# Optimization experiments

Hardware: AMD Instinct MI355X
Metric: run time of the kernel (lower is better)

Reference implementation:

```python
import jax, jax.numpy as jnp
import numpy as np

N, D = 8192, 512
LOGIT_SCALE = 2.659


def setup_inputs() -> dict:
    key = jax.random.key(0)
    k1, k2, k3 = jax.random.split(key, 3)
    text_features = jax.random.normal(k1, (N, D), dtype=jnp.float32)
    image_features = jax.random.normal(k2, (N, D), dtype=jnp.float32)
    labels = jax.random.randint(k3, (N,), 0, 100, dtype=jnp.int64)
    # sprinkle in some -1 (unlabeled) entries like the original supports
    labels = jnp.where(jax.random.uniform(jax.random.fold_in(key, 7), (N,)) < 0.1, -1, labels)
    return {"text_features": text_features, "image_features": image_features, "labels": labels}


def _l2_normalize(x):
    n = jnp.sqrt(jnp.sum(x * x, axis=-1, keepdims=True))
    return x / jnp.maximum(n, 1e-12)


def _soft_ce(s, t):
    # -(t * log softmax(s)).sum(-1) / t.sum(-1), averaged over rows
    loss = -jnp.sum(t * jax.nn.log_softmax(s, axis=-1), axis=-1)
    return jnp.mean(loss / jnp.sum(t, axis=-1))


def reference(text_features, image_features, labels):
    img = _l2_normalize(image_features)
    txt = _l2_normalize(text_features)
    logits_per_image = LOGIT_SCALE * (img @ txt.T)   # [N, N]
    logits_per_text = LOGIT_SCALE * (txt @ img.T)    # [N, N]

    # Vectorized equivalent of the per-row loop:
    # T[i,j] = 1 if i == j else (labels[i] == labels[j] and labels[i] != -1)
    eq = (labels[:, None] == labels[None, :]) & (labels[:, None] != -1)
    n = labels.shape[0]
    target = jnp.where(jnp.eye(n, dtype=bool), 1.0, eq.astype(jnp.float32))

    return (_soft_ce(logits_per_image, target) + _soft_ce(logits_per_text, target)) / 2
```

## Files before the change

### kernel.cpp

```cpp
#include <hip/hip_runtime.h>
#include <hip/hip_bf16.h>

#define N_ROWS 8192
#define DIM 512
#define SCALE 2.659f
#define MAXLOGIT 2.659f
#define LOG2E 1.4426950408889634f
#define NCHUNK 16
#define CHUNK 512
#define BM 128
#define BN 128
#define NCLS 128

typedef __attribute__((ext_vector_type(8))) short short8;
typedef __attribute__((ext_vector_type(4))) float f32x4;

#define ZERO_F4 36896

__device__ __forceinline__ unsigned short f2bf(float f) {
    unsigned int u = __float_as_uint(f);
    u += 0x7fffu + ((u >> 16) & 1u);
    return (unsigned short)(u >> 16);
}

__global__ __launch_bounds__(256) void norm_cast_kernel(
    const float* __restrict__ text, const float* __restrict__ image,
    const int* __restrict__ labels,
    unsigned short* __restrict__ imgn, unsigned short* __restrict__ txtn,
    float4* __restrict__ zbase, float* __restrict__ sd, float* __restrict__ out)
{
    int zi = blockIdx.x * 256 + threadIdx.x;
    if (zi < ZERO_F4) zbase[zi] = make_float4(0.f, 0.f, 0.f, 0.f);
    if (zi == 0) out[0] = 0.f;

    int row  = blockIdx.x * 4 + (threadIdx.x >> 6);
    int lane = threadIdx.x & 63;
    const float4* si = (const float4*)(image + (size_t)row * DIM) + lane * 2;
    const float4* st = (const float4*)(text  + (size_t)row * DIM) + lane * 2;
    float4 a = si[0], b = si[1], c = st[0], d = st[1];
    float ssa = a.x*a.x + a.y*a.y + a.z*a.z + a.w*a.w
              + b.x*b.x + b.y*b.y + b.z*b.z + b.w*b.w;
    float sst = c.x*c.x + c.y*c.y + c.z*c.z + c.w*c.w
              + d.x*d.x + d.y*d.y + d.z*d.z + d.w*d.w;
    float sab = a.x*c.x + a.y*c.y + a.z*c.z + a.w*c.w
              + b.x*d.x + b.y*d.y + b.z*d.z + b.w*d.w;
    #pragma unroll
    for (int m = 1; m < 64; m <<= 1) {
        ssa += __shfl_xor(ssa, m, 64);
        sst += __shfl_xor(sst, m, 64);
        sab += __shfl_xor(sab, m, 64);
    }
    float sca = 1.0f / fmaxf(sqrtf(ssa), 1e-12f);
    float sct = 1.0f / fmaxf(sqrtf(sst), 1e-12f);
    uint4 oi, ot;
    oi.x = (unsigned)f2bf(a.x*sca) | ((unsigned)f2bf(a.y*sca) << 16);
    oi.y = (unsigned)f2bf(a.z*sca) | ((unsigned)f2bf(a.w*sca) << 16);
    oi.z = (unsigned)f2bf(b.x*sca) | ((unsigned)f2bf(b.y*sca) << 16);
    oi.w = (unsigned)f2bf(b.z*sca) | ((unsigned)f2bf(b.w*sca) << 16);
    ot.x = (unsigned)f2bf(c.x*sct) | ((unsigned)f2bf(c.y*sct) << 16);
    ot.y = (unsigned)f2bf(c.z*sct) | ((unsigned)f2bf(c.w*sct) << 16);
    ot.z = (unsigned)f2bf(d.x*sct) | ((unsigned)f2bf(d.y*sct) << 16);
    ot.w = (unsigned)f2bf(d.z*sct) | ((unsigned)f2bf(d.w*sct) << 16);
    *((uint4*)(imgn + (size_t)row * DIM) + lane) = oi;
    *((uint4*)(txtn + (size_t)row * DIM) + lane) = ot;
    if (lane == 0)
        sd[row] = (labels[row] < 0) ? sab * sca * sct : 0.0f;
}

__global__ __launch_bounds__(256) void class_sum_kernel(
    const unsigned short* __restrict__ imgn, const unsigned short* __restrict__ txtn,
    const int* __restrict__ labels,
    float* __restrict__ c_txt, float* __restrict__ c_img, int* __restrict__ cnt)
{
    __shared__ int list[1024];
    __shared__ int lcount;
    int blk = blockIdx.x;
    int cls = blk & (NCLS - 1);
    int mat = (blk >> 7) & 1;
    int slc = blk >> 8;
    const unsigned* src = (const unsigned*)(mat ? imgn : txtn);
    float* dst = mat ? c_img : c_txt;
    int tid = threadIdx.x;
    if (tid == 0) lcount = 0;
    __syncthreads();
    int base0 = slc * 1024;
    #pragma unroll
    for (int it = 0; it < 4; ++it) {
        int i  = base0 + it * 256 + tid;
        int lb = labels[i];
        if (lb == cls) { int s = atomicAdd(&lcount, 1); list[s] = i; }
    }
    __syncthreads();
    int m = lcount;
    if (m == 0) return;
    if (mat == 0 && tid == 0) atomicAdd(&cnt[cls], m);
    float a0 = 0.f, a1 = 0.f;
    int r = 0;
    for (; r + 4 <= m; r += 4) {
        unsigned u0 = src[(size_t)list[r]   * (DIM/2) + tid];
        unsigned u1 = src[(size_t)list[r+1] * (DIM/2) + tid];
        unsigned u2 = src[(size_t)list[r+2] * (DIM/2) + tid];
        unsigned u3 = src[(size_t)list[r+3] * (DIM/2) + tid];
        a0 += __uint_as_float((u0 & 0xffffu) << 16) + __uint_as_float((u1 & 0xffffu) << 16)
            + __uint_as_float((u2 & 0xffffu) << 16) + __uint_as_float((u3 & 0xffffu) << 16);
        a1 += __uint_as_float(u0 & 0xffff0000u) + __uint_as_float(u1 & 0xffff0000u)
            + __uint_as_float(u2 & 0xffff0000u) + __uint_as_float(u3 & 0xffff0000u);
    }
    for (; r < m; ++r) {
        unsigned u = src[(size_t)list[r] * (DIM/2) + tid];
        a0 += __uint_as_float((u & 0xffffu) << 16);
        a1 += __uint_as_float(u & 0xffff0000u);
    }
    unsafeAtomicAdd(&dst[(size_t)cls * DIM + tid*2],     a0);
    unsafeAtomicAdd(&dst[(size_t)cls * DIM + tid*2 + 1], a1);
}

#define ASYNC16(gp, lp) \
  __builtin_amdgcn_global_load_lds((const __attribute__((address_space(1))) void*)(gp), \
                                   (__attribute__((address_space(3))) void*)(lp), 16, 0, 0)

#define SFENCE __builtin_amdgcn_sched_barrier(0)

#define STAGE(b, tcol, k0)                                                    \
  {                                                                           \
    const unsigned short* Ap = A + (size_t)(rowBase + w*16 + srow) * DIM      \
                                 + (k0) + spart;                              \
    const unsigned short* Bp = B + (size_t)((tcol) + w*16 + srow) * DIM       \
                                 + (k0) + spart;                              \
    ASYNC16(Ap,            &Ald[b][(w*16) * 32]);                             \
    ASYNC16(Ap + 64 * DIM, &Ald[b][(64 + w*16) * 32]);                        \
    ASYNC16(Bp,            &Bld[b][(w*16) * 32]);                             \
    ASYNC16(Bp + 64 * DIM, &Bld[b][(64 + w*16) * 32]);                        \
  }

__global__ __launch_bounds__(256, 2) void gemm_fused_kernel(
    const unsigned short* __restrict__ imgn, const unsigned short* __restrict__ txtn,
    float* __restrict__ rs, float* __restrict__ cs)
{
    __shared__ unsigned short Ald[4][BM * 32];
    __shared__ unsigned short Bld[4][BN * 32];
    __shared__ float red[2][BM];
    __shared__ float colb[2][CHUNK];

    int bid    = blockIdx.x;
    int rowblk = bid & 63;
    int chunk  = bid >> 6;
    const unsigned short* A = imgn;
    const unsigned short* B = txtn;
    int rowBase  = rowblk * BM;
    int colBase0 = chunk * CHUNK;

    int tid  = threadIdx.x;
    int lane = tid & 63;
    int w    = tid >> 6;
    int wr   = w >> 1, wc = w & 1;
    int q    = lane >> 4;
    int lm   = lane & 15;

    float s_acc[16];
    #pragma unroll
    for (int i = 0; i < 16; ++i) s_acc[i] = 0.f;

    int srow  = lane >> 2;
    int spart = (lane & 3) * 8;

    const float C1 = SCALE * LOG2E;
    const float C2 = -MAXLOGIT * LOG2E;

    STAGE(0, colBase0, 0);
    STAGE(1, colBase0, 32);
    SFENCE;
    asm volatile("s_waitcnt vmcnt(4)" ::: "memory");
    SFENCE;
    __builtin_amdgcn_s_barrier();
    SFENCE;

    #pragma unroll 1
    for (int tile = 0; tile < CHUNK / BN; ++tile) {
        f32x4 acc[4][4];
        #pragma unroll
        for (int mi = 0; mi < 4; ++mi)
          #pragma unroll
          for (int ni = 0; ni < 4; ++ni)
            acc[mi][ni] = (f32x4){0.f, 0.f, 0.f, 0.f};

        #pragma unroll
        for (int kt = 0; kt < DIM / 32; ++kt) {
            const int bcur = kt & 3;
            const int bpf  = (kt + 2) & 3;
            int g2 = tile * 16 + kt + 2;
            if (g2 < 64) {
                int t2 = g2 >> 4, k2 = g2 & 15;
                STAGE(bpf, colBase0 + t2 * BN, k2 * 32);
            }

            short8 af[4], bf[4];
            #pragma unroll
            for (int mi = 0; mi < 4; ++mi)
                af[mi] = *(const short8*)(&Ald[bcur][(wr*64 + mi*16 + lm)*32 + q*8]);
            #pragma unroll
            for (int ni = 0; ni < 4; ++ni)
                bf[ni] = *(const short8*)(&Bld[bcur][(wc*64 + ni*16 + lm)*32 + q*8]);
            #pragma unroll
            for (int mi = 0; mi < 4; ++mi)
              #pragma unroll
              for (int ni = 0; ni < 4; ++ni)
                acc[mi][ni] = __builtin_amdgcn_mfma_f32_16x16x32_bf16(
                                  af[mi], bf[ni], acc[mi][ni], 0, 0, 0);

            if (kt == DIM / 32 - 1) {
                #pragma unroll
                for (int ni = 0; ni < 4; ++ni) {
                    float csum = 0.f;
                    #pragma unroll
                    for (int mi = 0; mi < 4; ++mi) {
                      #pragma unroll
                      for (int r = 0; r < 4; ++r) {
                        float e = __builtin_amdgcn_exp2f(fmaf(acc[mi][ni][r], C1, C2));
                        s_acc[mi*4 + r] += e;
                        csum += e;
                      }
                    }
                    csum += __shfl_xor(csum, 16, 64);
                    csum += __shfl_xor(csum, 32, 64);
                    if (q == 0)
                        colb[wr][tile*BN + wc*64 + ni*16 + lm] = csum;
                }
            }

            SFENCE;
            if (g2 < 64) asm volatile("s_waitcnt vmcnt(4)" ::: "memory");
            else         asm volatile("s_waitcnt vmcnt(0)" ::: "memory");
            SFENCE;
            __builtin_amdgcn_s_barrier();
            SFENCE;
        }
    }

    #pragma unroll
    for (int idx = 0; idx < 16; ++idx) {
        float s = s_acc[idx];
        #pragma unroll
        for (int m = 1; m < 16; m <<= 1) s += __shfl_xor(s, m, 64);
        s_acc[idx] = s;
    }
    if (lm == 0) {
        #pragma unroll
        for (int idx = 0; idx < 16; ++idx) {
            int rl = wr*64 + (idx>>2)*16 + q*4 + (idx&3);
            red[wc][rl] = s_acc[idx];
        }
    }
    __syncthreads();
    if (tid < BM)
        unsafeAtomicAdd(&rs[rowBase + tid], red[0][tid] + red[1][tid]);
    for (int c = tid; c < CHUNK; c += 256)
        unsafeAtomicAdd(&cs[colBase0 + c], colb[0][c] + colb[1][c]);
}

__global__ __launch_bounds__(256) void loss_tail_kernel(
    const float* __restrict__ rs, const float* __restrict__ cs,
    const float* __restrict__ sd, const float* __restrict__ c_txt,
    const float* __restrict__ c_img, const int* __restrict__ cnt,
    float* __restrict__ out)
{
    __shared__ float wsum[4];
    int tid = threadIdx.x, lane = tid & 63, w = tid >> 6;
    int gidx = blockIdx.x * 256 + tid;
    float local;
    if (gidx < N_ROWS)
        local = (MAXLOGIT + logf(rs[gidx])) - 2.0f * SCALE * sd[gidx];
    else
        local = MAXLOGIT + logf(cs[gidx - N_ROWS]);

    int cls = blockIdx.x * 2 + (tid >> 7);
    int e0  = (tid & 127) * 4;
    int n   = cnt[cls];
    if (n > 0) {
        float4 x = *(const float4*)(c_txt + (size_t)cls * DIM + e0);
        float4 y = *(const float4*)(c_img + (size_t)cls * DIM + e0);
        float dotp = x.x*y.x + x.y*y.y + x.z*y.z + x.w*y.w;
        local -= 2.0f * SCALE * dotp / (float)n;
    }

    #pragma unroll
    for (int m = 1; m < 64; m <<= 1) local += __shfl_xor(local, m, 64);
    if (lane == 0) wsum[w] = local;
    __syncthreads();
    if (tid == 0)
        unsafeAtomicAdd(out, (wsum[0] + wsum[1] + wsum[2] + wsum[3])
                             * (1.0f / (2 * N_ROWS)));
}

extern "C" void kernel_launch(void* const* d_in, const int* in_sizes, int n_in,
                              void* d_out, int out_size, void* d_ws, size_t ws_size,
                              hipStream_t stream)
{
    const float* text   = (const float*)d_in[0];
    const float* image  = (const float*)d_in[1];
    const int*   labels = (const int*)d_in[2];

    unsigned short* imgn = (unsigned short*)d_ws;
    unsigned short* txtn = imgn + (size_t)N_ROWS * DIM;
    char* p = (char*)d_ws + 2 * (size_t)N_ROWS * DIM * sizeof(unsigned short);
    float* rs    = (float*)p;
    float* cs    = rs + N_ROWS;
    float* c_txt = cs + N_ROWS;
    float* c_img = c_txt + (size_t)NCLS * DIM;
    int*   cnt   = (int*)(c_img + (size_t)NCLS * DIM);
    float* sd    = (float*)(cnt + NCLS);
    float* out = (float*)d_out;

    hipLaunchKernelGGL(norm_cast_kernel, dim3(N_ROWS / 4), dim3(256), 0, stream,
                       text, image, labels, imgn, txtn, (float4*)rs, sd, out);
    hipLaunchKernelGGL(gemm_fused_kernel, dim3(64 * NCHUNK), dim3(256), 0, stream,
                       imgn, txtn, rs, cs);
    hipLaunchKernelGGL(class_sum_kernel, dim3(16 * NCLS), dim3(256), 0, stream,
                       imgn, txtn, labels, c_txt, c_img, cnt);
    hipLaunchKernelGGL(loss_tail_kernel, dim3(64), dim3(256), 0, stream,
                       rs, cs, sd, c_txt, c_img, cnt, out);
}
```

Baseline: 171.0 us.

## Use 256x256 GEMM tiles and fold class-sum work into the GEMM launch

```diff
diff --git a/kernel.cpp b/kernel.cpp
--- a/kernel.cpp
+++ b/kernel.cpp
@@ -6,11 +6,10 @@
 #define SCALE 2.659f
 #define MAXLOGIT 2.659f
 #define LOG2E 1.4426950408889634f
-#define NCHUNK 16
-#define CHUNK 512
-#define BM 128
-#define BN 128
+#define BM 256
+#define BN 256
 #define NCLS 128
+#define GEMM_BLKS 1024
 
 typedef __attribute__((ext_vector_type(8))) short short8;
 typedef __attribute__((ext_vector_type(4))) float f32x4;
@@ -67,195 +66,180 @@
         sd[row] = (labels[row] < 0) ? sab * sca * sct : 0.0f;
 }
 
-__global__ __launch_bounds__(256) void class_sum_kernel(
-    const unsigned short* __restrict__ imgn, const unsigned short* __restrict__ txtn,
-    const int* __restrict__ labels,
-    float* __restrict__ c_txt, float* __restrict__ c_img, int* __restrict__ cnt)
-{
-    __shared__ int list[1024];
-    __shared__ int lcount;
-    int blk = blockIdx.x;
-    int cls = blk & (NCLS - 1);
-    int mat = (blk >> 7) & 1;
-    int slc = blk >> 8;
-    const unsigned* src = (const unsigned*)(mat ? imgn : txtn);
-    float* dst = mat ? c_img : c_txt;
-    int tid = threadIdx.x;
-    if (tid == 0) lcount = 0;
-    __syncthreads();
-    int base0 = slc * 1024;
-    #pragma unroll
-    for (int it = 0; it < 4; ++it) {
-        int i  = base0 + it * 256 + tid;
-        int lb = labels[i];
-        if (lb == cls) { int s = atomicAdd(&lcount, 1); list[s] = i; }
-    }
-    __syncthreads();
-    int m = lcount;
-    if (m == 0) return;
-    if (mat == 0 && tid == 0) atomicAdd(&cnt[cls], m);
-    float a0 = 0.f, a1 = 0.f;
-    int r = 0;
-    for (; r + 4 <= m; r += 4) {
-        unsigned u0 = src[(size_t)list[r]   * (DIM/2) + tid];
-        unsigned u1 = src[(size_t)list[r+1] * (DIM/2) + tid];
-        unsigned u2 = src[(size_t)list[r+2] * (DIM/2) + tid];
-        unsigned u3 = src[(size_t)list[r+3] * (DIM/2) + tid];
-        a0 += __uint_as_float((u0 & 0xffffu) << 16) + __uint_as_float((u1 & 0xffffu) << 16)
-            + __uint_as_float((u2 & 0xffffu) << 16) + __uint_as_float((u3 & 0xffffu) << 16);
-        a1 += __uint_as_float(u0 & 0xffff0000u) + __uint_as_float(u1 & 0xffff0000u)
-            + __uint_as_float(u2 & 0xffff0000u) + __uint_as_float(u3 & 0xffff0000u);
-    }
-    for (; r < m; ++r) {
-        unsigned u = src[(size_t)list[r] * (DIM/2) + tid];
-        a0 += __uint_as_float((u & 0xffffu) << 16);
-        a1 += __uint_as_float(u & 0xffff0000u);
-    }
-    unsafeAtomicAdd(&dst[(size_t)cls * DIM + tid*2],     a0);
-    unsafeAtomicAdd(&dst[(size_t)cls * DIM + tid*2 + 1], a1);
-}
-
 #define ASYNC16(gp, lp) \
   __builtin_amdgcn_global_load_lds((const __attribute__((address_space(1))) void*)(gp), \
                                    (__attribute__((address_space(3))) void*)(lp), 16, 0, 0)
 
 #define SFENCE __builtin_amdgcn_sched_barrier(0)
 
-#define STAGE(b, tcol, k0)                                                    \
+#define STAGE(b, k0)                                                          \
   {                                                                           \
     const unsigned short* Ap = A + (size_t)(rowBase + w*16 + srow) * DIM      \
                                  + (k0) + spart;                              \
-    const unsigned short* Bp = B + (size_t)((tcol) + w*16 + srow) * DIM       \
+    const unsigned short* Bp = B + (size_t)(colBase + w*16 + srow) * DIM      \
                                  + (k0) + spart;                              \
-    ASYNC16(Ap,            &Ald[b][(w*16) * 32]);                             \
-    ASYNC16(Ap + 64 * DIM, &Ald[b][(64 + w*16) * 32]);                        \
-    ASYNC16(Bp,            &Bld[b][(w*16) * 32]);                             \
-    ASYNC16(Bp + 64 * DIM, &Bld[b][(64 + w*16) * 32]);                        \
+    ASYNC16(Ap,             &Ald[b][(w*16) * 32]);                            \
+    ASYNC16(Ap + 128 * DIM, &Ald[b][(128 + w*16) * 32]);                      \
+    ASYNC16(Bp,             &Bld[b][(w*16) * 32]);                            \
+    ASYNC16(Bp + 128 * DIM, &Bld[b][(128 + w*16) * 32]);                      \
   }
 
-__global__ __launch_bounds__(256, 2) void gemm_fused_kernel(
+__global__ __launch_bounds__(512, 2) void gemm_fused_kernel(
     const unsigned short* __restrict__ imgn, const unsigned short* __restrict__ txtn,
-    float* __restrict__ rs, float* __restrict__ cs)
+    const int* __restrict__ labels,
+    float* __restrict__ rs, float* __restrict__ cs,
+    float* __restrict__ c_txt, float* __restrict__ c_img, int* __restrict__ cnt)
 {
     __shared__ unsigned short Ald[4][BM * 32];
     __shared__ unsigned short Bld[4][BN * 32];
-    __shared__ float red[2][BM];
-    __shared__ float colb[2][CHUNK];
+    __shared__ float red[4][BM];
+    __shared__ float colb[2][BN];
+    __shared__ int   list[1024];
+    __shared__ int   lcount;
+
+    int tid  = threadIdx.x;
+
+    if (blockIdx.x >= GEMM_BLKS) {
+        int blk = blockIdx.x - GEMM_BLKS;
+        int cls = blk & (NCLS - 1);
+        int mat = blk >> 7;
+        const unsigned* src = (const unsigned*)(mat ? imgn : txtn);
+        float* dst = mat ? c_img : c_txt;
+        if (tid == 0) lcount = 0;
+        __syncthreads();
+        #pragma unroll
+        for (int base = 0; base < N_ROWS; base += 512) {
+            int lb = labels[base + tid];
+            if (lb == cls) { int s = atomicAdd(&lcount, 1); list[s & 1023] = base + tid; }
+        }
+        __syncthreads();
+        int m = lcount;
+        if (mat == 0 && tid == 0) cnt[cls] = m;
+        int half = tid >> 8;
+        int col  = tid & 255;
+        float a0 = 0.f, a1 = 0.f;
+        int r = half;
+        for (; r + 6 < m; r += 8) {
+            unsigned u0 = src[(size_t)list[r]   * (DIM/2) + col];
+            unsigned u1 = src[(size_t)list[r+2] * (DIM/2) + col];
+            unsigned u2 = src[(size_t)list[r+4] * (DIM/2) + col];
+            unsigned u3 = src[(size_t)list[r+6] * (DIM/2) + col];
+            a0 += __uint_as_float((u0 & 0xffffu) << 16) + __uint_as_float((u1 & 0xffffu) << 16)
+                + __uint_as_float((u2 & 0xffffu) << 16) + __uint_as_float((u3 & 0xffffu) << 16);
+            a1 += __uint_as_float(u0 & 0xffff0000u) + __uint_as_float(u1 & 0xffff0000u)
+                + __uint_as_float(u2 & 0xffff0000u) + __uint_as_float(u3 & 0xffff0000u);
+        }
+        for (; r < m; r += 2) {
+            unsigned u = src[(size_t)list[r] * (DIM/2) + col];
+            a0 += __uint_as_float((u & 0xffffu) << 16);
+            a1 += __uint_as_float(u & 0xffff0000u);
+        }
+        if (a0 != 0.f || a1 != 0.f) {
+            unsafeAtomicAdd(&dst[(size_t)cls * DIM + col*2],     a0);
+            unsafeAtomicAdd(&dst[(size_t)cls * DIM + col*2 + 1], a1);
+        }
+        return;
+    }
 
     int bid    = blockIdx.x;
-    int rowblk = bid & 63;
-    int chunk  = bid >> 6;
+    int rowblk = bid & 31;
+    int colblk = bid >> 5;
     const unsigned short* A = imgn;
     const unsigned short* B = txtn;
-    int rowBase  = rowblk * BM;
-    int colBase0 = chunk * CHUNK;
-
-    int tid  = threadIdx.x;
+    int rowBase = rowblk * BM;
+    int colBase = colblk * BN;
+
     int lane = tid & 63;
     int w    = tid >> 6;
-    int wr   = w >> 1, wc = w & 1;
+    int wr   = w >> 2, wc = w & 3;
     int q    = lane >> 4;
     int lm   = lane & 15;
 
-    float s_acc[16];
-    #pragma unroll
-    for (int i = 0; i < 16; ++i) s_acc[i] = 0.f;
-
     int srow  = lane >> 2;
     int spart = (lane & 3) * 8;
 
     const float C1 = SCALE * LOG2E;
     const float C2 = -MAXLOGIT * LOG2E;
 
-    STAGE(0, colBase0, 0);
-    STAGE(1, colBase0, 32);
+    f32x4 acc[8][4];
+    #pragma unroll
+    for (int mi = 0; mi < 8; ++mi)
+      #pragma unroll
+      for (int ni = 0; ni < 4; ++ni)
+        acc[mi][ni] = (f32x4){0.f, 0.f, 0.f, 0.f};
+
+    STAGE(0, 0);
+    STAGE(1, 32);
     SFENCE;
     asm volatile("s_waitcnt vmcnt(4)" ::: "memory");
     SFENCE;
     __builtin_amdgcn_s_barrier();
     SFENCE;
 
-    #pragma unroll 1
-    for (int tile = 0; tile < CHUNK / BN; ++tile) {
-        f32x4 acc[4][4];
-        #pragma unroll
-        for (int mi = 0; mi < 4; ++mi)
+    #pragma unroll
+    for (int g = 0; g < DIM / 32; ++g) {
+        const int bcur = g & 3;
+        const int bpf  = (g + 2) & 3;
+        if (g + 2 < DIM / 32) {
+            STAGE(bpf, (g + 2) * 32);
+        }
+
+        short8 af[8], bf[4];
+        #pragma unroll
+        for (int mi = 0; mi < 8; ++mi)
+            af[mi] = *(const short8*)(&Ald[bcur][(wr*128 + mi*16 + lm)*32 + q*8]);
+        #pragma unroll
+        for (int ni = 0; ni < 4; ++ni)
+            bf[ni] = *(const short8*)(&Bld[bcur][(wc*64 + ni*16 + lm)*32 + q*8]);
+        #pragma unroll
+        for (int mi = 0; mi < 8; ++mi)
           #pragma unroll
           for (int ni = 0; ni < 4; ++ni)
-            acc[mi][ni] = (f32x4){0.f, 0.f, 0.f, 0.f};
-
-        #pragma unroll
-        for (int kt = 0; kt < DIM / 32; ++kt) {
-            const int bcur = kt & 3;
-            const int bpf  = (kt + 2) & 3;
-            int g2 = tile * 16 + kt + 2;
-            if (g2 < 64) {
-                int t2 = g2 >> 4, k2 = g2 & 15;
-                STAGE(bpf, colBase0 + t2 * BN, k2 * 32);
-            }
-
-            short8 af[4], bf[4];
-            #pragma unroll
-            for (int mi = 0; mi < 4; ++mi)
-                af[mi] = *(const short8*)(&Ald[bcur][(wr*64 + mi*16 + lm)*32 + q*8]);
-            #pragma unroll
-            for (int ni = 0; ni < 4; ++ni)
-                bf[ni] = *(const short8*)(&Bld[bcur][(wc*64 + ni*16 + lm)*32 + q*8]);
-            #pragma unroll
-            for (int mi = 0; mi < 4; ++mi)
-              #pragma unroll
-              for (int ni = 0; ni < 4; ++ni)
-                acc[mi][ni] = __builtin_amdgcn_mfma_f32_16x16x32_bf16(
-                                  af[mi], bf[ni], acc[mi][ni], 0, 0, 0);
-
-            if (kt == DIM / 32 - 1) {
-                #pragma unroll
-                for (int ni = 0; ni < 4; ++ni) {
-                    float csum = 0.f;
-                    #pragma unroll
-                    for (int mi = 0; mi < 4; ++mi) {
-                      #pragma unroll
-                      for (int r = 0; r < 4; ++r) {
-                        float e = __builtin_amdgcn_exp2f(fmaf(acc[mi][ni][r], C1, C2));
-                        s_acc[mi*4 + r] += e;
-                        csum += e;
-                      }
-                    }
-                    csum += __shfl_xor(csum, 16, 64);
-                    csum += __shfl_xor(csum, 32, 64);
-                    if (q == 0)
-                        colb[wr][tile*BN + wc*64 + ni*16 + lm] = csum;
-                }
-            }
-
-            SFENCE;
-            if (g2 < 64) asm volatile("s_waitcnt vmcnt(4)" ::: "memory");
-            else         asm volatile("s_waitcnt vmcnt(0)" ::: "memory");
-            SFENCE;
-            __builtin_amdgcn_s_barrier();
-            SFENCE;
-        }
-    }
-
-    #pragma unroll
-    for (int idx = 0; idx < 16; ++idx) {
-        float s = s_acc[idx];
+            acc[mi][ni] = __builtin_amdgcn_mfma_f32_16x16x32_bf16(
+                              af[mi], bf[ni], acc[mi][ni], 0, 0, 0);
+
+        SFENCE;
+        if (g + 2 < DIM / 32) asm volatile("s_waitcnt vmcnt(4)" ::: "memory");
+        else                  asm volatile("s_waitcnt vmcnt(0)" ::: "memory");
+        SFENCE;
+        __builtin_amdgcn_s_barrier();
+        SFENCE;
+    }
+
+    float rsum[32];
+    #pragma unroll
+    for (int i = 0; i < 32; ++i) rsum[i] = 0.f;
+    #pragma unroll
+    for (int ni = 0; ni < 4; ++ni) {
+        float csum = 0.f;
+        #pragma unroll
+        for (int mi = 0; mi < 8; ++mi) {
+          #pragma unroll
+          for (int r = 0; r < 4; ++r) {
+            float e = __builtin_amdgcn_exp2f(fmaf(acc[mi][ni][r], C1, C2));
+            rsum[mi*4 + r] += e;
+            csum += e;
+          }
+        }
+        csum += __shfl_xor(csum, 16, 64);
+        csum += __shfl_xor(csum, 32, 64);
+        if (q == 0)
+            colb[wr][wc*64 + ni*16 + lm] = csum;
+    }
+    #pragma unroll
+    for (int idx = 0; idx < 32; ++idx) {
+        float s = rsum[idx];
         #pragma unroll
         for (int m = 1; m < 16; m <<= 1) s += __shfl_xor(s, m, 64);
-        s_acc[idx] = s;
-    }
-    if (lm == 0) {
-        #pragma unroll
-        for (int idx = 0; idx < 16; ++idx) {
-            int rl = wr*64 + (idx>>2)*16 + q*4 + (idx&3);
-            red[wc][rl] = s_acc[idx];
-        }
+        if (lm == 0)
+            red[wc][wr*128 + (idx>>2)*16 + q*4 + (idx&3)] = s;
     }
     __syncthreads();
-    if (tid < BM)
-        unsafeAtomicAdd(&rs[rowBase + tid], red[0][tid] + red[1][tid]);
-    for (int c = tid; c < CHUNK; c += 256)
-        unsafeAtomicAdd(&cs[colBase0 + c], colb[0][c] + colb[1][c]);
+    if (tid < BM) {
+        unsafeAtomicAdd(&rs[rowBase + tid],
+                        red[0][tid] + red[1][tid] + red[2][tid] + red[3][tid]);
+        unsafeAtomicAdd(&cs[colBase + tid], colb[0][tid] + colb[1][tid]);
+    }
 }
 
 __global__ __launch_bounds__(256) void loss_tail_kernel(
@@ -313,10 +297,8 @@
 
     hipLaunchKernelGGL(norm_cast_kernel, dim3(N_ROWS / 4), dim3(256), 0, stream,
                        text, image, labels, imgn, txtn, (float4*)rs, sd, out);
-    hipLaunchKernelGGL(gemm_fused_kernel, dim3(64 * NCHUNK), dim3(256), 0, stream,
-                       imgn, txtn, rs, cs);
-    hipLaunchKernelGGL(class_sum_kernel, dim3(16 * NCLS), dim3(256), 0, stream,
-                       imgn, txtn, labels, c_txt, c_img, cnt);
+    hipLaunchKernelGGL(gemm_fused_kernel, dim3(GEMM_BLKS + 2 * NCLS), dim3(512), 0, stream,
+                       imgn, txtn, labels, rs, cs, c_txt, c_img, cnt);
     hipLaunchKernelGGL(loss_tail_kernel, dim3(64), dim3(256), 0, stream,
                        rs, cs, sd, c_txt, c_img, cnt, out);
 }
```

Result: no change. 168.2 us (-1.7%).

## Merge class-sum blocks into GEMM launch and XOR-swizzle LDS tiles

Applied to the files above, without the earlier changes.

```diff
diff --git a/kernel.cpp b/kernel.cpp
--- a/kernel.cpp
+++ b/kernel.cpp
@@ -11,6 +11,7 @@
 #define BM 128
 #define BN 128
 #define NCLS 128
+#define GEMM_BLKS 1024
 
 typedef __attribute__((ext_vector_type(8))) short short8;
 typedef __attribute__((ext_vector_type(4))) float f32x4;
@@ -67,54 +68,6 @@
         sd[row] = (labels[row] < 0) ? sab * sca * sct : 0.0f;
 }
 
-__global__ __launch_bounds__(256) void class_sum_kernel(
-    const unsigned short* __restrict__ imgn, const unsigned short* __restrict__ txtn,
-    const int* __restrict__ labels,
-    float* __restrict__ c_txt, float* __restrict__ c_img, int* __restrict__ cnt)
-{
-    __shared__ int list[1024];
-    __shared__ int lcount;
-    int blk = blockIdx.x;
-    int cls = blk & (NCLS - 1);
-    int mat = (blk >> 7) & 1;
-    int slc = blk >> 8;
-    const unsigned* src = (const unsigned*)(mat ? imgn : txtn);
-    float* dst = mat ? c_img : c_txt;
-    int tid = threadIdx.x;
-    if (tid == 0) lcount = 0;
-    __syncthreads();
-    int base0 = slc * 1024;
-    #pragma unroll
-    for (int it = 0; it < 4; ++it) {
-        int i  = base0 + it * 256 + tid;
-        int lb = labels[i];
-        if (lb == cls) { int s = atomicAdd(&lcount, 1); list[s] = i; }
-    }
-    __syncthreads();
-    int m = lcount;
-    if (m == 0) return;
-    if (mat == 0 && tid == 0) atomicAdd(&cnt[cls], m);
-    float a0 = 0.f, a1 = 0.f;
-    int r = 0;
-    for (; r + 4 <= m; r += 4) {
-        unsigned u0 = src[(size_t)list[r]   * (DIM/2) + tid];
-        unsigned u1 = src[(size_t)list[r+1] * (DIM/2) + tid];
-        unsigned u2 = src[(size_t)list[r+2] * (DIM/2) + tid];
-        unsigned u3 = src[(size_t)list[r+3] * (DIM/2) + tid];
-        a0 += __uint_as_float((u0 & 0xffffu) << 16) + __uint_as_float((u1 & 0xffffu) << 16)
-            + __uint_as_float((u2 & 0xffffu) << 16) + __uint_as_float((u3 & 0xffffu) << 16);
-        a1 += __uint_as_float(u0 & 0xffff0000u) + __uint_as_float(u1 & 0xffff0000u)
-            + __uint_as_float(u2 & 0xffff0000u) + __uint_as_float(u3 & 0xffff0000u);
-    }
-    for (; r < m; ++r) {
-        unsigned u = src[(size_t)list[r] * (DIM/2) + tid];
-        a0 += __uint_as_float((u & 0xffffu) << 16);
-        a1 += __uint_as_float(u & 0xffff0000u);
-    }
-    unsafeAtomicAdd(&dst[(size_t)cls * DIM + tid*2],     a0);
-    unsafeAtomicAdd(&dst[(size_t)cls * DIM + tid*2 + 1], a1);
-}
-
 #define ASYNC16(gp, lp) \
   __builtin_amdgcn_global_load_lds((const __attribute__((address_space(1))) void*)(gp), \
                                    (__attribute__((address_space(3))) void*)(lp), 16, 0, 0)
@@ -124,9 +77,9 @@
 #define STAGE(b, tcol, k0)                                                    \
   {                                                                           \
     const unsigned short* Ap = A + (size_t)(rowBase + w*16 + srow) * DIM      \
-                                 + (k0) + spart;                              \
+                                 + (k0) + spsw;                               \
     const unsigned short* Bp = B + (size_t)((tcol) + w*16 + srow) * DIM       \
-                                 + (k0) + spart;                              \
+                                 + (k0) + spsw;                               \
     ASYNC16(Ap,            &Ald[b][(w*16) * 32]);                             \
     ASYNC16(Ap + 64 * DIM, &Ald[b][(64 + w*16) * 32]);                        \
     ASYNC16(Bp,            &Bld[b][(w*16) * 32]);                             \
@@ -135,12 +88,60 @@
 
 __global__ __launch_bounds__(256, 2) void gemm_fused_kernel(
     const unsigned short* __restrict__ imgn, const unsigned short* __restrict__ txtn,
-    float* __restrict__ rs, float* __restrict__ cs)
+    const int* __restrict__ labels,
+    float* __restrict__ rs, float* __restrict__ cs,
+    float* __restrict__ c_txt, float* __restrict__ c_img, int* __restrict__ cnt)
 {
     __shared__ unsigned short Ald[4][BM * 32];
     __shared__ unsigned short Bld[4][BN * 32];
     __shared__ float red[2][BM];
     __shared__ float colb[2][CHUNK];
+    __shared__ int   list[1024];
+    __shared__ int   lcount;
+
+    int tid  = threadIdx.x;
+
+    if (blockIdx.x >= GEMM_BLKS) {
+        int blk = blockIdx.x - GEMM_BLKS;
+        int cls = blk & (NCLS - 1);
+        int mat = (blk >> 7) & 1;
+        int slc = blk >> 8;
+        const unsigned* src = (const unsigned*)(mat ? imgn : txtn);
+        float* dst = mat ? c_img : c_txt;
+        if (tid == 0) lcount = 0;
+        __syncthreads();
+        int base0 = slc * 1024;
+        #pragma unroll
+        for (int it = 0; it < 4; ++it) {
+            int i  = base0 + it * 256 + tid;
+            int lb = labels[i];
+            if (lb == cls) { int s = atomicAdd(&lcount, 1); list[s & 1023] = i; }
+        }
+        __syncthreads();
+        int m = lcount;
+        if (m == 0) return;
+        if (mat == 0 && tid == 0) atomicAdd(&cnt[cls], m);
+        float a0 = 0.f, a1 = 0.f;
+        int r = 0;
+        for (; r + 4 <= m; r += 4) {
+            unsigned u0 = src[(size_t)list[r]   * (DIM/2) + tid];
+            unsigned u1 = src[(size_t)list[r+1] * (DIM/2) + tid];
+            unsigned u2 = src[(size_t)list[r+2] * (DIM/2) + tid];
+            unsigned u3 = src[(size_t)list[r+3] * (DIM/2) + tid];
+            a0 += __uint_as_float((u0 & 0xffffu) << 16) + __uint_as_float((u1 & 0xffffu) << 16)
+                + __uint_as_float((u2 & 0xffffu) << 16) + __uint_as_float((u3 & 0xffffu) << 16);
+            a1 += __uint_as_float(u0 & 0xffff0000u) + __uint_as_float(u1 & 0xffff0000u)
+                + __uint_as_float(u2 & 0xffff0000u) + __uint_as_float(u3 & 0xffff0000u);
+        }
+        for (; r < m; ++r) {
+            unsigned u = src[(size_t)list[r] * (DIM/2) + tid];
+            a0 += __uint_as_float((u & 0xffffu) << 16);
+            a1 += __uint_as_float(u & 0xffff0000u);
+        }
+        unsafeAtomicAdd(&dst[(size_t)cls * DIM + tid*2],     a0);
+        unsafeAtomicAdd(&dst[(size_t)cls * DIM + tid*2 + 1], a1);
+        return;
+    }
 
     int bid    = blockIdx.x;
     int rowblk = bid & 63;
@@ -150,19 +151,19 @@
     int rowBase  = rowblk * BM;
     int colBase0 = chunk * CHUNK;
 
-    int tid  = threadIdx.x;
     int lane = tid & 63;
     int w    = tid >> 6;
     int wr   = w >> 1, wc = w & 1;
     int q    = lane >> 4;
     int lm   = lane & 15;
+    int qa   = q ^ ((lm >> 1) & 3);
 
     float s_acc[16];
     #pragma unroll
     for (int i = 0; i < 16; ++i) s_acc[i] = 0.f;
 
-    int srow  = lane >> 2;
-    int spart = (lane & 3) * 8;
+    int srow = lane >> 2;
+    int spsw = (((lane & 3) ^ ((lane >> 3) & 3)) * 8);
 
     const float C1 = SCALE * LOG2E;
     const float C2 = -MAXLOGIT * LOG2E;
@@ -197,10 +198,10 @@
             short8 af[4], bf[4];
             #pragma unroll
             for (int mi = 0; mi < 4; ++mi)
-                af[mi] = *(const short8*)(&Ald[bcur][(wr*64 + mi*16 + lm)*32 + q*8]);
+                af[mi] = *(const short8*)(&Ald[bcur][(wr*64 + mi*16 + lm)*32 + qa*8]);
             #pragma unroll
             for (int ni = 0; ni < 4; ++ni)
-                bf[ni] = *(const short8*)(&Bld[bcur][(wc*64 + ni*16 + lm)*32 + q*8]);
+                bf[ni] = *(const short8*)(&Bld[bcur][(wc*64 + ni*16 + lm)*32 + qa*8]);
             #pragma unroll
             for (int mi = 0; mi < 4; ++mi)
               #pragma unroll
@@ -313,10 +314,8 @@
 
     hipLaunchKernelGGL(norm_cast_kernel, dim3(N_ROWS / 4), dim3(256), 0, stream,
                        text, image, labels, imgn, txtn, (float4*)rs, sd, out);
-    hipLaunchKernelGGL(gemm_fused_kernel, dim3(64 * NCHUNK), dim3(256), 0, stream,
-                       imgn, txtn, rs, cs);
-    hipLaunchKernelGGL(class_sum_kernel, dim3(16 * NCLS), dim3(256), 0, stream,
-                       imgn, txtn, labels, c_txt, c_img, cnt);
+    hipLaunchKernelGGL(gemm_fused_kernel, dim3(GEMM_BLKS + 2048), dim3(256), 0, stream,
+                       imgn, txtn, labels, rs, cs, c_txt, c_img, cnt);
     hipLaunchKernelGGL(loss_tail_kernel, dim3(64), dim3(256), 0, stream,
                        rs, cs, sd, c_txt, c_img, cnt, out);
 }
```

New measurement: 167.4 us, median of 2. 1.02x faster.
